# Kernel tuning notes

Hardware: AMD Instinct MI355X
Metric: run time of the kernel (lower is better)

The kernel has to match this reference:

```python
import jax, jax.numpy as jnp
import numpy as np

D_MODEL = 1024
N_HEADS = 16
HEAD_DIM = D_MODEL // N_HEADS
SCALE = HEAD_DIM ** -0.5


def setup_inputs() -> dict:
    key = jax.random.key(0)
    ks = jax.random.split(key, 5)
    B, T = 2, 2048
    w_std = D_MODEL ** -0.5  # ~ torch Linear init scale
    return {
        "x": jax.random.normal(ks[0], (B, T, D_MODEL), dtype=jnp.float32),
        "W_q": jax.random.normal(ks[1], (D_MODEL, D_MODEL), dtype=jnp.float32) * w_std,
        "W_k": jax.random.normal(ks[2], (D_MODEL, D_MODEL), dtype=jnp.float32) * w_std,
        "W_v": jax.random.normal(ks[3], (D_MODEL, D_MODEL), dtype=jnp.float32) * w_std,
        "W_o": jax.random.normal(ks[4], (D_MODEL, D_MODEL), dtype=jnp.float32) * w_std,
    }


def reference(x, W_q, W_k, W_v, W_o):
    # torch Linear: y = x @ W.T  (weight stored as (out, in))
    B, T, _ = x.shape

    def split_heads(y):  # (B,T,D) -> (B,H,T,hd)
        return y.reshape(B, T, N_HEADS, HEAD_DIM).transpose(0, 2, 1, 3)

    q = split_heads(x @ W_q.T)
    k = split_heads(x @ W_k.T)
    v = split_heads(x @ W_v.T)

    attn = jnp.einsum("bhqd,bhkd->bhqk", q, k) * SCALE  # (B,H,T,T)
    attn = jax.nn.softmax(attn, axis=-1)
    out = jnp.einsum("bhqk,bhkd->bhqd", attn, v)  # (B,H,T,hd)
    out = out.transpose(0, 2, 1, 3).reshape(B, T, D_MODEL)
    return out @ W_o.T
```

## Files before the change

kernel.cpp:

```cpp
#include <hip/hip_runtime.h>
#include <hip/hip_bf16.h>

#define D_MODEL 1024
#define N_HEADS 16
#define HEAD_DIM 64
#define SEQ 2048
#define BATCH 2

typedef __attribute__((ext_vector_type(8))) short bf16x8;
typedef __attribute__((ext_vector_type(4))) float f32x4;
typedef __attribute__((ext_vector_type(16))) float f32x16;

typedef __attribute__((address_space(3))) unsigned lds_uint;
typedef __attribute__((address_space(1))) const unsigned global_cuint;

__device__ __forceinline__ void async_cp16(const ushort* g, ushort* l) {
  __builtin_amdgcn_global_load_lds((global_cuint*)g, (lds_uint*)l, 16, 0, 0);
}

__device__ __forceinline__ ushort f2b(float f) {
  union { float f; unsigned u; } x; x.f = f;
  unsigned r = x.u + 0x7fffu + ((x.u >> 16) & 1u);
  return (ushort)(r >> 16);
}

__device__ __forceinline__ unsigned pk2(float a, float b) {
  __hip_bfloat162 h = __float22bfloat162_rn(float2{a, b});
  union { __hip_bfloat162 h; unsigned u; } x; x.h = h;
  return x.u;
}

__device__ __forceinline__ float blo(unsigned u) {
  union { unsigned u; float f; } x; x.u = u << 16; return x.f;
}
__device__ __forceinline__ float bhi(unsigned u) {
  union { unsigned u; float f; } x; x.u = u & 0xffff0000u; return x.f;
}

__device__ __forceinline__ int swz64(int row, int colbyte) {
  return row * 64 + ((colbyte ^ ((row & 7) << 4)) >> 1);
}

__global__ __launch_bounds__(256) void cast_all(const float* __restrict__ x,
                                                const float* __restrict__ Wq,
                                                const float* __restrict__ Wk,
                                                const float* __restrict__ Wv,
                                                const float* __restrict__ Wo,
                                                ushort* __restrict__ xb,
                                                ushort* __restrict__ wqkv,
                                                ushort* __restrict__ wob) {
  int idx = blockIdx.x * 256 + threadIdx.x;
  const float* in;
  uint2* out;
  if (idx < (1 << 20)) {
    in = x; out = (uint2*)xb;
  } else {
    int j = idx - (1 << 20);
    int w = j >> 18;
    idx = j & 0x3FFFF;
    switch (w) {
      case 0: in = Wq; out = (uint2*)wqkv; break;
      case 1: in = Wk; out = (uint2*)(wqkv) + (1 << 18); break;
      case 2: in = Wv; out = (uint2*)(wqkv) + (2 << 18); break;
      default: in = Wo; out = (uint2*)wob; break;
    }
  }
  float4 v = ((const float4*)in)[idx];
  uint2 o; o.x = pk2(v.x, v.y); o.y = pk2(v.z, v.w);
  out[idx] = o;
}

__global__ __launch_bounds__(256) void gemm_qkv(const ushort* __restrict__ A,
                                                const ushort* __restrict__ Bw,
                                                ushort* __restrict__ Qh,
                                                ushort* __restrict__ Kh,
                                                ushort* __restrict__ Vth,
                                                float qscale) {
  constexpr int K = 1024;
  const int bm = blockIdx.y * 128;
  const int bn = blockIdx.x * 128;
  const int tid = threadIdx.x;
  const int wave = tid >> 6;
  const int lane = tid & 63;
  const int l16 = lane & 15;
  const int quad = lane >> 4;

  __shared__ ushort As[2][128 * 64];
  __shared__ ushort Bs[2][128 * 64];

  const int wm = (wave & 1) * 64;
  const int wn = (wave >> 1) * 64;

  f32x4 acc[4][4];
#pragma unroll
  for (int r = 0; r < 4; ++r)
#pragma unroll
    for (int c = 0; c < 4; ++c) acc[r][c] = (f32x4){0.f, 0.f, 0.f, 0.f};

  const int srow = wave * 8 + (lane >> 3);
  const int csw = (((lane & 7) ^ (lane >> 3)) << 3);

#pragma unroll
  for (int j = 0; j < 4; ++j) {
    async_cp16(A  + (size_t)(bm + j * 32 + srow) * K + csw, &As[0][(j * 32 + wave * 8) * 64]);
    async_cp16(Bw + (size_t)(bn + j * 32 + srow) * K + csw, &Bs[0][(j * 32 + wave * 8) * 64]);
  }

  constexpr int NIT = K / 64;
  for (int kt = 0; kt < NIT; ++kt) {
    __syncthreads();
    const int buf = kt & 1;
    if (kt + 1 < NIT) {
      const int k0 = (kt + 1) * 64;
#pragma unroll
      for (int j = 0; j < 4; ++j) {
        async_cp16(A  + (size_t)(bm + j * 32 + srow) * K + k0 + csw, &As[buf ^ 1][(j * 32 + wave * 8) * 64]);
        async_cp16(Bw + (size_t)(bn + j * 32 + srow) * K + k0 + csw, &Bs[buf ^ 1][(j * 32 + wave * 8) * 64]);
      }
    }

    bf16x8 a[2][4], b[2][4];
#pragma unroll
    for (int ks = 0; ks < 2; ++ks)
#pragma unroll
      for (int r = 0; r < 4; ++r) {
        a[ks][r] = *(const bf16x8*)(&As[buf][swz64(wm + r * 16 + l16, ks * 64 + quad * 16)]);
        b[ks][r] = *(const bf16x8*)(&Bs[buf][swz64(wn + r * 16 + l16, ks * 64 + quad * 16)]);
      }
#pragma unroll
    for (int ks = 0; ks < 2; ++ks)
#pragma unroll
      for (int r = 0; r < 4; ++r)
#pragma unroll
        for (int c = 0; c < 4; ++c)
          acc[r][c] = __builtin_amdgcn_mfma_f32_16x16x32_bf16(a[ks][r], b[ks][c], acc[r][c], 0, 0, 0);
  }

#pragma unroll
  for (int r = 0; r < 4; ++r) {
#pragma unroll
    for (int c = 0; c < 4; ++c) {
      int ncol = bn + wn + c * 16 + l16;
      int w = ncol >> 10;
      int f = ncol & 1023;
      int h = f >> 6, d = f & 63;
      if (w == 2) {
        int m0 = bm + wm + r * 16 + quad * 4;
        int b = m0 >> 11, t0 = m0 & 2047;
        uint2 pp;
        pp.x = pk2(acc[r][c][0], acc[r][c][1]);
        pp.y = pk2(acc[r][c][2], acc[r][c][3]);
        *(uint2*)(&Vth[((size_t)(b * 1024 + f) << 11) + t0]) = pp;
      } else {
#pragma unroll
        for (int rr = 0; rr < 4; ++rr) {
          float v = acc[r][c][rr];
          int m = bm + wm + r * 16 + quad * 4 + rr;
          int b = m >> 11, t = m & 2047;
          if (w == 0)
            Qh[((size_t)(b * 16 + h) * SEQ + t) * 64 + d] = f2b(v * qscale);
          else
            Kh[((size_t)(b * 16 + h) * SEQ + t) * 64 + d] = f2b(v);
        }
      }
    }
  }
}

__global__ __launch_bounds__(256) void gemm_out(const ushort* __restrict__ A,
                                                const ushort* __restrict__ Bw,
                                                float* __restrict__ out) {
  constexpr int K = 1024;
  const int bm = blockIdx.y * 64;
  const int bn = blockIdx.x * 128;
  const int tid = threadIdx.x;
  const int wave = tid >> 6;
  const int lane = tid & 63;
  const int l16 = lane & 15;
  const int quad = lane >> 4;

  __shared__ ushort As[2][64 * 64];
  __shared__ ushort Bs[2][128 * 64];

  const int wm = (wave & 1) * 32;
  const int wn = (wave >> 1) * 64;

  f32x4 acc[2][4];
#pragma unroll
  for (int r = 0; r < 2; ++r)
#pragma unroll
    for (int c = 0; c < 4; ++c) acc[r][c] = (f32x4){0.f, 0.f, 0.f, 0.f};

  const int srow = wave * 8 + (lane >> 3);
  const int csw = (((lane & 7) ^ (lane >> 3)) << 3);

#pragma unroll
  for (int j = 0; j < 2; ++j)
    async_cp16(A + (size_t)(bm + j * 32 + srow) * K + csw, &As[0][(j * 32 + wave * 8) * 64]);
#pragma unroll
  for (int j = 0; j < 4; ++j)
    async_cp16(Bw + (size_t)(bn + j * 32 + srow) * K + csw, &Bs[0][(j * 32 + wave * 8) * 64]);

  constexpr int NIT = K / 64;
  for (int kt = 0; kt < NIT; ++kt) {
    __syncthreads();
    const int buf = kt & 1;
    if (kt + 1 < NIT) {
      const int k0 = (kt + 1) * 64;
#pragma unroll
      for (int j = 0; j < 2; ++j)
        async_cp16(A + (size_t)(bm + j * 32 + srow) * K + k0 + csw, &As[buf ^ 1][(j * 32 + wave * 8) * 64]);
#pragma unroll
      for (int j = 0; j < 4; ++j)
        async_cp16(Bw + (size_t)(bn + j * 32 + srow) * K + k0 + csw, &Bs[buf ^ 1][(j * 32 + wave * 8) * 64]);
    }

    bf16x8 a[2][2], b[2][4];
#pragma unroll
    for (int ks = 0; ks < 2; ++ks) {
#pragma unroll
      for (int r = 0; r < 2; ++r)
        a[ks][r] = *(const bf16x8*)(&As[buf][swz64(wm + r * 16 + l16, ks * 64 + quad * 16)]);
#pragma unroll
      for (int c = 0; c < 4; ++c)
        b[ks][c] = *(const bf16x8*)(&Bs[buf][swz64(wn + c * 16 + l16, ks * 64 + quad * 16)]);
    }
#pragma unroll
    for (int ks = 0; ks < 2; ++ks)
#pragma unroll
      for (int r = 0; r < 2; ++r)
#pragma unroll
        for (int c = 0; c < 4; ++c)
          acc[r][c] = __builtin_amdgcn_mfma_f32_16x16x32_bf16(a[ks][r], b[ks][c], acc[r][c], 0, 0, 0);
  }

#pragma unroll
  for (int r = 0; r < 2; ++r)
#pragma unroll
    for (int c = 0; c < 4; ++c)
#pragma unroll
      for (int rr = 0; rr < 4; ++rr) {
        int m = bm + wm + r * 16 + quad * 4 + rr;
        int n = bn + wn + c * 16 + l16;
        out[(size_t)m * D_MODEL + n] = acc[r][c][rr];
      }
}

__global__ __launch_bounds__(256, 2) void attn_kernel(const ushort* __restrict__ Qh,
                                                      const ushort* __restrict__ Kh,
                                                      const ushort* __restrict__ Vth,
                                                      ushort* __restrict__ O1,
                                                      ushort* __restrict__ O2,
                                                      ushort* __restrict__ O3,
                                                      ushort* __restrict__ O4,
                                                      float* __restrict__ l1,
                                                      float* __restrict__ l2,
                                                      float* __restrict__ l3,
                                                      float* __restrict__ l4) {
  const int id = blockIdx.x;
  const int stream = id & 127;
  const int qb = id >> 7;
  const int bh = stream >> 2;
  const int quarter = stream & 3;
  const int q0 = qb * 128;
  ushort* __restrict__ Op = (quarter == 0) ? O1 : (quarter == 1) ? O2 : (quarter == 2) ? O3 : O4;
  float* __restrict__ lp = (quarter == 0) ? l1 : (quarter == 1) ? l2 : (quarter == 2) ? l3 : l4;

  const int tid = threadIdx.x;
  const int wave = tid >> 6;
  const int lane = tid & 63;
  const int l31 = lane & 31;
  const int hi = lane >> 5;

  __shared__ ushort KVbuf[2][2][64 * 64];

  bf16x8 qf[4];
#pragma unroll
  for (int dc = 0; dc < 4; ++dc)
    qf[dc] = *(const bf16x8*)(Qh + ((size_t)bh * SEQ + q0 + wave * 32 + l31) * 64 + dc * 16 + hi * 8);

  f32x16 o0 = {0.f, 0.f, 0.f, 0.f, 0.f, 0.f, 0.f, 0.f,
               0.f, 0.f, 0.f, 0.f, 0.f, 0.f, 0.f, 0.f};
  f32x16 o1 = o0;
  float lacc = 0.f;

  const int chunk = wave * 2;
  const int r8 = lane >> 3;
  const int csw = (((lane & 7) ^ r8) << 3);
  const ushort* kbase = Kh + ((size_t)bh * SEQ + quarter * 512) * 64;
  const ushort* vbase = Vth + (size_t)bh * 64 * SEQ + quarter * 512;
  const ushort* ksrc = kbase + (size_t)(chunk * 8 + r8) * 64 + csw;
  const ushort* vsrc = vbase + (size_t)(chunk * 8 + r8) * SEQ + csw;

  async_cp16(ksrc,           &KVbuf[0][0][chunk * 512]);
  async_cp16(ksrc + 8 * 64,  &KVbuf[0][0][(chunk + 1) * 512]);
  async_cp16(vsrc,           &KVbuf[0][1][chunk * 512]);
  async_cp16(vsrc + 8 * SEQ, &KVbuf[0][1][(chunk + 1) * 512]);

  constexpr int NIT = 512 / 64;
  for (int kt = 0; kt < NIT; ++kt) {
    __syncthreads();
    const int buf = kt & 1;
    if (kt + 1 < NIT) {
      const ushort* ks = ksrc + (size_t)(kt + 1) * 64 * 64;
      const ushort* vs = vsrc + (kt + 1) * 64;
      async_cp16(ks,           &KVbuf[buf ^ 1][0][chunk * 512]);
      async_cp16(ks + 8 * 64,  &KVbuf[buf ^ 1][0][(chunk + 1) * 512]);
      async_cp16(vs,           &KVbuf[buf ^ 1][1][chunk * 512]);
      async_cp16(vs + 8 * SEQ, &KVbuf[buf ^ 1][1][(chunk + 1) * 512]);
    }
    const ushort* Kt = KVbuf[buf][0];
    const ushort* Vt = KVbuf[buf][1];

#pragma unroll
    for (int kt2 = 0; kt2 < 2; ++kt2) {
      bf16x8 ka0 = *(const bf16x8*)(&Kt[swz64(kt2 * 32 + l31, 0 * 32 + hi * 16)]);
      bf16x8 ka1 = *(const bf16x8*)(&Kt[swz64(kt2 * 32 + l31, 1 * 32 + hi * 16)]);
      bf16x8 ka2 = *(const bf16x8*)(&Kt[swz64(kt2 * 32 + l31, 2 * 32 + hi * 16)]);
      bf16x8 ka3 = *(const bf16x8*)(&Kt[swz64(kt2 * 32 + l31, 3 * 32 + hi * 16)]);
      f32x16 z = {0.f, 0.f, 0.f, 0.f, 0.f, 0.f, 0.f, 0.f,
                  0.f, 0.f, 0.f, 0.f, 0.f, 0.f, 0.f, 0.f};
      z = __builtin_amdgcn_mfma_f32_32x32x16_bf16(ka0, qf[0], z, 0, 0, 0);
      z = __builtin_amdgcn_mfma_f32_32x32x16_bf16(ka1, qf[1], z, 0, 0, 0);
      z = __builtin_amdgcn_mfma_f32_32x32x16_bf16(ka2, qf[2], z, 0, 0, 0);
      z = __builtin_amdgcn_mfma_f32_32x32x16_bf16(ka3, qf[3], z, 0, 0, 0);

      float e[16];
#pragma unroll
      for (int r = 0; r < 16; ++r) e[r] = __builtin_amdgcn_exp2f(z[r]);
      lacc += (((e[0] + e[1]) + (e[2] + e[3])) + ((e[4] + e[5]) + (e[6] + e[7])))
            + (((e[8] + e[9]) + (e[10] + e[11])) + ((e[12] + e[13]) + (e[14] + e[15])));

#pragma unroll
      for (int lw = 0; lw < 2; ++lw) {
        const int base = lw * 8;
        unsigned pa0 = pk2(e[base + 0], e[base + 1]);
        unsigned pa1 = pk2(e[base + 2], e[base + 3]);
        unsigned pa2 = pk2(e[base + 4], e[base + 5]);
        unsigned pa3 = pk2(e[base + 6], e[base + 7]);
        unsigned s0 = hi ? pa0 : pa2;
        unsigned s1 = hi ? pa1 : pa3;
        unsigned t0 = __shfl_xor(s0, 32, 64);
        unsigned t1 = __shfl_xor(s1, 32, 64);
        pa2 = hi ? pa2 : t0;
        pa3 = hi ? pa3 : t1;
        pa0 = hi ? t0 : pa0;
        pa1 = hi ? t1 : pa1;
        union { unsigned u[4]; bf16x8 v; } pu;
        pu.u[0] = pa0; pu.u[1] = pa1; pu.u[2] = pa2; pu.u[3] = pa3;
        const int wb = (kt2 * 2 + lw) * 32;
        bf16x8 vb0 = *(const bf16x8*)(&Vt[swz64(0 + l31, wb + hi * 16)]);
        bf16x8 vb1 = *(const bf16x8*)(&Vt[swz64(32 + l31, wb + hi * 16)]);
        o0 = __builtin_amdgcn_mfma_f32_32x32x16_bf16(pu.v, vb0, o0, 0, 0, 0);
        o1 = __builtin_amdgcn_mfma_f32_32x32x16_bf16(pu.v, vb1, o1, 0, 0, 0);
      }
    }
  }

  {
    float ltot = lacc + __shfl_xor(lacc, 32, 64);
    if (hi == 0)
      lp[(size_t)bh * SEQ + q0 + wave * 32 + l31] = ltot;
  }

  __syncthreads();
  ushort* Ob = &KVbuf[0][0][0];
#pragma unroll
  for (int r = 0; r < 16; ++r) {
    int row = wave * 32 + (r & 3) + 8 * (r >> 2) + 4 * hi;
    Ob[row * 64 + l31] = f2b(o0[r]);
    Ob[row * 64 + 32 + l31] = f2b(o1[r]);
  }
  __syncthreads();
  {
    uint4* dst = (uint4*)(Op + ((size_t)bh * SEQ + q0) * 64);
    const uint4* src = (const uint4*)Ob;
#pragma unroll
    for (int i = 0; i < 4; ++i)
      dst[i * 256 + tid] = src[i * 256 + tid];
  }
}

__global__ __launch_bounds__(256) void recombine(const ushort* __restrict__ O1,
                                                 const ushort* __restrict__ O2,
                                                 const ushort* __restrict__ O3,
                                                 const ushort* __restrict__ O4,
                                                 const float* __restrict__ l1,
                                                 const float* __restrict__ l2,
                                                 const float* __restrict__ l3,
                                                 const float* __restrict__ l4,
                                                 ushort* __restrict__ ctx) {
  int idx = blockIdx.x * 256 + threadIdx.x;
  int row = idx >> 3;
  int d8 = idx & 7;
  uint4 a = ((const uint4*)O1)[idx];
  uint4 b = ((const uint4*)O2)[idx];
  uint4 c = ((const uint4*)O3)[idx];
  uint4 d = ((const uint4*)O4)[idx];
  float linv = 1.f / (((l1[row] + l2[row]) + (l3[row] + l4[row])));
  uint4 res;
  unsigned* ap = (unsigned*)&a;
  unsigned* bp = (unsigned*)&b;
  unsigned* cp = (unsigned*)&c;
  unsigned* dp = (unsigned*)&d;
  unsigned* rp = (unsigned*)&res;
#pragma unroll
  for (int i = 0; i < 4; ++i) {
    float lo = ((blo(ap[i]) + blo(bp[i])) + (blo(cp[i]) + blo(dp[i]))) * linv;
    float hi = ((bhi(ap[i]) + bhi(bp[i])) + (bhi(cp[i]) + bhi(dp[i]))) * linv;
    rp[i] = pk2(lo, hi);
  }
  int bh = row >> 11, t = row & 2047;
  int bb = bh >> 4, h = bh & 15;
  ((uint4*)ctx)[(size_t)(bb * SEQ + t) * 128 + h * 8 + d8] = res;
}

extern "C" void kernel_launch(void* const* d_in, const int* in_sizes, int n_in,
                              void* d_out, int out_size, void* d_ws, size_t ws_size,
                              hipStream_t stream) {
  const float* x  = (const float*)d_in[0];
  const float* Wq = (const float*)d_in[1];
  const float* Wk = (const float*)d_in[2];
  const float* Wv = (const float*)d_in[3];
  const float* Wo = (const float*)d_in[4];
  float* out = (float*)d_out;

  char* ws = (char*)d_ws;
  const size_t MB = 1 << 20;
  ushort* xb   = (ushort*)(ws);
  ushort* wqkv = (ushort*)(ws +  8 * MB);
  ushort* wob  = (ushort*)(ws + 14 * MB);
  ushort* Qh   = (ushort*)(ws + 16 * MB);
  ushort* Kh   = (ushort*)(ws + 24 * MB);
  ushort* Vth  = (ushort*)(ws + 32 * MB);
  ushort* ctxO = (ushort*)(ws + 40 * MB);

  ushort* O1 = (ushort*)d_out;
  ushort* O2 = xb;
  ushort* O3 = ctxO;
  ushort* O4 = (ushort*)d_out + (4u << 20);
  float*  l1 = (float*)wqkv;
  float*  l2 = (float*)(ws + 8 * MB + 256 * 1024);
  float*  l3 = (float*)(ws + 8 * MB + 512 * 1024);
  float*  l4 = (float*)(ws + 8 * MB + 768 * 1024);
  ushort* ctx = Qh;

  cast_all<<<8192, 256, 0, stream>>>(x, Wq, Wk, Wv, Wo, xb, wqkv, wob);

  const float qscale = 0.125f * 1.44269504089f;
  gemm_qkv<<<dim3(3072 / 128, 4096 / 128), 256, 0, stream>>>(xb, wqkv, Qh, Kh, Vth, qscale);

  attn_kernel<<<(SEQ / 128) * BATCH * N_HEADS * 4, 256, 0, stream>>>(
      Qh, Kh, Vth, O1, O2, O3, O4, l1, l2, l3, l4);

  recombine<<<(BATCH * N_HEADS * SEQ * 64 / 8) / 256, 256, 0, stream>>>(
      O1, O2, O3, O4, l1, l2, l3, l4, ctx);

  gemm_out<<<dim3(1024 / 128, 4096 / 64), 256, 0, stream>>>(ctx, wob, out);
}
```

Before: 200.6 us.

## Load V tiles directly from global into registers, keep only K in LDS

V is no longer staged through double-buffered shared memory. Each wave loads its V fragments straight from global memory into registers inside the inner loop, and only K stays in LDS. K read offsets are also precomputed once instead of being recomputed per iteration. The aim is to halve LDS footprint and traffic and drop the async V copies. The cost is strided, poorly coalesced global loads that every wave repeats, and these loads sit on the critical path without prefetching.

New measurement: 222.2 us. 1.11x slower.

```diff
diff --git a/kernel.cpp b/kernel.cpp
--- a/kernel.cpp
+++ b/kernel.cpp
@@ -272,7 +272,7 @@
   const int l31 = lane & 31;
   const int hi = lane >> 5;
 
-  __shared__ ushort KVbuf[2][2][64 * 64];
+  __shared__ ushort Kbuf[2][64 * 64];
 
   bf16x8 qf[4];
 #pragma unroll
@@ -290,12 +290,16 @@
   const ushort* kbase = Kh + ((size_t)bh * SEQ + quarter * 512) * 64;
   const ushort* vbase = Vth + (size_t)bh * 64 * SEQ + quarter * 512;
   const ushort* ksrc = kbase + (size_t)(chunk * 8 + r8) * 64 + csw;
-  const ushort* vsrc = vbase + (size_t)(chunk * 8 + r8) * SEQ + csw;
-
-  async_cp16(ksrc,           &KVbuf[0][0][chunk * 512]);
-  async_cp16(ksrc + 8 * 64,  &KVbuf[0][0][(chunk + 1) * 512]);
-  async_cp16(vsrc,           &KVbuf[0][1][chunk * 512]);
-  async_cp16(vsrc + 8 * SEQ, &KVbuf[0][1][(chunk + 1) * 512]);
+
+  int koff[2][4];
+#pragma unroll
+  for (int kt2 = 0; kt2 < 2; ++kt2)
+#pragma unroll
+    for (int dc = 0; dc < 4; ++dc)
+      koff[kt2][dc] = swz64(kt2 * 32 + l31, dc * 32 + hi * 16);
+
+  async_cp16(ksrc,          &Kbuf[0][chunk * 512]);
+  async_cp16(ksrc + 8 * 64, &Kbuf[0][(chunk + 1) * 512]);
 
   constexpr int NIT = 512 / 64;
   for (int kt = 0; kt < NIT; ++kt) {
@@ -303,21 +307,23 @@
     const int buf = kt & 1;
     if (kt + 1 < NIT) {
       const ushort* ks = ksrc + (size_t)(kt + 1) * 64 * 64;
-      const ushort* vs = vsrc + (kt + 1) * 64;
-      async_cp16(ks,           &KVbuf[buf ^ 1][0][chunk * 512]);
-      async_cp16(ks + 8 * 64,  &KVbuf[buf ^ 1][0][(chunk + 1) * 512]);
-      async_cp16(vs,           &KVbuf[buf ^ 1][1][chunk * 512]);
-      async_cp16(vs + 8 * SEQ, &KVbuf[buf ^ 1][1][(chunk + 1) * 512]);
-    }
-    const ushort* Kt = KVbuf[buf][0];
-    const ushort* Vt = KVbuf[buf][1];
+      async_cp16(ks,          &Kbuf[buf ^ 1][chunk * 512]);
+      async_cp16(ks + 8 * 64, &Kbuf[buf ^ 1][(chunk + 1) * 512]);
+    }
+    const ushort* Kt = Kbuf[buf];
 
 #pragma unroll
     for (int kt2 = 0; kt2 < 2; ++kt2) {
-      bf16x8 ka0 = *(const bf16x8*)(&Kt[swz64(kt2 * 32 + l31, 0 * 32 + hi * 16)]);
-      bf16x8 ka1 = *(const bf16x8*)(&Kt[swz64(kt2 * 32 + l31, 1 * 32 + hi * 16)]);
-      bf16x8 ka2 = *(const bf16x8*)(&Kt[swz64(kt2 * 32 + l31, 2 * 32 + hi * 16)]);
-      bf16x8 ka3 = *(const bf16x8*)(&Kt[swz64(kt2 * 32 + l31, 3 * 32 + hi * 16)]);
+      const ushort* vt = vbase + kt * 64 + kt2 * 32 + hi * 8;
+      bf16x8 v00 = *(const bf16x8*)(vt + (size_t)l31 * SEQ);
+      bf16x8 v01 = *(const bf16x8*)(vt + (size_t)l31 * SEQ + 16);
+      bf16x8 v10 = *(const bf16x8*)(vt + (size_t)(32 + l31) * SEQ);
+      bf16x8 v11 = *(const bf16x8*)(vt + (size_t)(32 + l31) * SEQ + 16);
+
+      bf16x8 ka0 = *(const bf16x8*)(Kt + koff[kt2][0]);
+      bf16x8 ka1 = *(const bf16x8*)(Kt + koff[kt2][1]);
+      bf16x8 ka2 = *(const bf16x8*)(Kt + koff[kt2][2]);
+      bf16x8 ka3 = *(const bf16x8*)(Kt + koff[kt2][3]);
       f32x16 z = {0.f, 0.f, 0.f, 0.f, 0.f, 0.f, 0.f, 0.f,
                   0.f, 0.f, 0.f, 0.f, 0.f, 0.f, 0.f, 0.f};
       z = __builtin_amdgcn_mfma_f32_32x32x16_bf16(ka0, qf[0], z, 0, 0, 0);
@@ -348,11 +354,8 @@
         pa1 = hi ? t1 : pa1;
         union { unsigned u[4]; bf16x8 v; } pu;
         pu.u[0] = pa0; pu.u[1] = pa1; pu.u[2] = pa2; pu.u[3] = pa3;
-        const int wb = (kt2 * 2 + lw) * 32;
-        bf16x8 vb0 = *(const bf16x8*)(&Vt[swz64(0 + l31, wb + hi * 16)]);
-        bf16x8 vb1 = *(const bf16x8*)(&Vt[swz64(32 + l31, wb + hi * 16)]);
-        o0 = __builtin_amdgcn_mfma_f32_32x32x16_bf16(pu.v, vb0, o0, 0, 0, 0);
-        o1 = __builtin_amdgcn_mfma_f32_32x32x16_bf16(pu.v, vb1, o1, 0, 0, 0);
+        o0 = __builtin_amdgcn_mfma_f32_32x32x16_bf16(pu.v, lw ? v01 : v00, o0, 0, 0, 0);
+        o1 = __builtin_amdgcn_mfma_f32_32x32x16_bf16(pu.v, lw ? v11 : v10, o1, 0, 0, 0);
       }
     }
   }
@@ -364,7 +367,7 @@
   }
 
   __syncthreads();
-  ushort* Ob = &KVbuf[0][0][0];
+  ushort* Ob = &Kbuf[0][0];
 #pragma unroll
   for (int r = 0; r < 16; ++r) {
     int row = wave * 32 + (r & 3) + 8 * (r >> 2) + 4 * hi;
```
